# Optimization experiments

Measured on AMD Instinct MI355X. Metric: run time of the kernel, lower is better.

The kernel has to match this reference:

```python
import jax, jax.numpy as jnp
import numpy as np

N = 50000      # nodes
E = 800000     # edges (avg degree 16)
IN = 128
H = 128
OUT = 64
L = 3          # num GIN layers
G = 512        # graphs in batch
BN_EPS = 1e-5


def setup_inputs() -> dict:
    key = jax.random.key(0)
    ks = jax.random.split(key, 16)
    x = jax.random.normal(ks[0], (N, IN), dtype=jnp.float32)
    edge_index = jax.random.randint(ks[1], (2, E), 0, N, dtype=jnp.int64)
    batch = jnp.sort(jax.random.randint(ks[2], (N,), 0, G, dtype=jnp.int64))

    s_in = 1.0 / np.sqrt(IN)
    s_h = 1.0 / np.sqrt(H)
    # layer 0 has fan-in IN == H so we can stack all L layers uniformly
    conv_W1 = jax.random.normal(ks[3], (L, IN, H), dtype=jnp.float32) * s_in
    conv_b1 = jnp.zeros((L, H), dtype=jnp.float32)
    conv_gamma = jnp.ones((L, H), dtype=jnp.float32)
    conv_beta = jnp.zeros((L, H), dtype=jnp.float32)
    conv_W2 = jax.random.normal(ks[4], (L, H, H), dtype=jnp.float32) * s_h
    conv_b2 = jnp.zeros((L, H), dtype=jnp.float32)

    head_W1 = jax.random.normal(ks[5], (H, H), dtype=jnp.float32) * s_h
    head_b1 = jnp.zeros((H,), dtype=jnp.float32)
    head_W2 = jax.random.normal(ks[6], (H, OUT), dtype=jnp.float32) * s_h
    head_b2 = jnp.zeros((OUT,), dtype=jnp.float32)

    return dict(x=x, conv_W1=conv_W1, conv_b1=conv_b1, conv_gamma=conv_gamma,
                conv_beta=conv_beta, conv_W2=conv_W2, conv_b2=conv_b2,
                head_W1=head_W1, head_b1=head_b1, head_W2=head_W2,
                head_b2=head_b2, edge_index=edge_index, batch=batch)


def _mlp_bn(h, W1, b1, gamma, beta, W2, b2):
    # Linear -> BatchNorm (batch stats, biased var) -> ReLU -> Linear
    h = h @ W1 + b1
    mu = jnp.mean(h, axis=0)
    var = jnp.var(h, axis=0)
    h = (h - mu) * jax.lax.rsqrt(var + BN_EPS) * gamma + beta
    h = jax.nn.relu(h)
    return h @ W2 + b2


def reference(x, conv_W1, conv_b1, conv_gamma, conv_beta, conv_W2, conv_b2,
              head_W1, head_b1, head_W2, head_b2, edge_index, batch):
    src, dst = edge_index[0], edge_index[1]
    for l in range(L):
        # GINConv, eps=0: nn(x_i + sum_{j->i} x_j)
        agg = jax.ops.segment_sum(x[src], dst, num_segments=N)
        x = jax.nn.relu(_mlp_bn(x + agg, conv_W1[l], conv_b1[l],
                                conv_gamma[l], conv_beta[l],
                                conv_W2[l], conv_b2[l]))
    # global_add_pool -> [G, H]
    g = jax.ops.segment_sum(x, batch, num_segments=G)
    # head MLP (norm=None, dropout eval-mode identity)
    g = jax.nn.relu(g @ head_W1 + head_b1)
    return g @ head_W2 + head_b2
```

## Files before the change

kernel.cpp:

```cpp
#include <hip/hip_runtime.h>

#define N_NODES 50000
#define N_EDGES 800000
#define HDIM 128
#define ODIM 64
#define NLAYER 3
#define NGRAPH 512
#define BN_EPS 1e-5f
#define BCAP 48
#define NBUCKET 256
#define BRANGE 196
#define NBLK 782
#define GBLK 782
#define PROWS 64
#define HPITCH 136
#define TPITCH 136

#define SCAT_BLK 782
#define CVT_BLK 6250
#define CVTW_BLK 673

typedef __attribute__((ext_vector_type(8))) short short8;
typedef __attribute__((ext_vector_type(8))) unsigned short ushort8;
typedef __attribute__((ext_vector_type(4))) unsigned char uchar4x;
typedef __attribute__((ext_vector_type(2))) unsigned int uint2x;
typedef __attribute__((ext_vector_type(2))) float floatx2;
typedef __attribute__((ext_vector_type(4))) float floatx4;

static __device__ __forceinline__ unsigned short f2bf(float f) {
    union { float f; unsigned int u; } v; v.f = f;
    unsigned int r = v.u + 0x7FFFu + ((v.u >> 16) & 1u);
    return (unsigned short)(r >> 16);
}
static __device__ __forceinline__ float bf2f(unsigned short s) {
    union { unsigned int u; float f; } v; v.u = ((unsigned int)s) << 16;
    return v.f;
}
static __device__ __forceinline__ unsigned char f2e4(float f) {
    union { float f; unsigned int u; } v; v.f = f;
    unsigned char s = (unsigned char)((v.u >> 24) & 0x80u);
    float a = fabsf(f);
    if (a >= 448.f) return (unsigned char)(s | 0x7Eu);
    if (a < 0.015625f) return s;
    v.f = a;
    unsigned int r = v.u + 0x7FFFFu + ((v.u >> 20) & 1u);
    int e8 = (int)((r >> 23) & 0xFF) - 127 + 7;
    unsigned int man = (r >> 20) & 0x7u;
    if (e8 <= 0) return s;
    if (e8 > 15) return (unsigned char)(s | 0x7Eu);
    return (unsigned char)(s | ((unsigned)e8 << 3) | man);
}
static __device__ __forceinline__ void acc8_fp8(float* acc, const unsigned char* p) {
    uint2x u = *(const uint2x*)p;
    floatx2 p0 = __builtin_amdgcn_cvt_pk_f32_fp8(u[0], false);
    floatx2 p1 = __builtin_amdgcn_cvt_pk_f32_fp8(u[0], true);
    floatx2 p2 = __builtin_amdgcn_cvt_pk_f32_fp8(u[1], false);
    floatx2 p3 = __builtin_amdgcn_cvt_pk_f32_fp8(u[1], true);
    acc[0] += p0[0]; acc[1] += p0[1]; acc[2] += p1[0]; acc[3] += p1[1];
    acc[4] += p2[0]; acc[5] += p2[1]; acc[6] += p3[0]; acc[7] += p3[1];
}


__global__ __launch_bounds__(256) void k_prep(
    const int* __restrict__ src, const int* __restrict__ dst,
    unsigned int* __restrict__ bstore,
    unsigned int* __restrict__ prefW,
    int* __restrict__ vcnt,
    const float* __restrict__ x, unsigned char* __restrict__ xa,
    const float* __restrict__ W1, const float* __restrict__ W2,
    const float* __restrict__ hW1, const float* __restrict__ hW2,
    unsigned short* __restrict__ wtb,
    float* __restrict__ p64all)
{
    int b = blockIdx.x;
    int tid = threadIdx.x;
    if (b < SCAT_BLK) {
        __shared__ int hist[NBUCKET], pos[NBUCKET];
        __shared__ int sa[NBUCKET], sb[NBUCKET];
        __shared__ unsigned int sed[1024];
        hist[tid] = 0;
        __syncthreads();

        int base = (b * 256 + tid) * 4;
        bool valid = base < N_EDGES;
        unsigned int ev[4]; int bk[4];
        if (valid) {
            int4 s4 = *(const int4*)(src + base);
            int4 d4 = *(const int4*)(dst + base);
            ev[0] = (unsigned)s4.x | ((unsigned)d4.x << 16); bk[0] = d4.x / BRANGE;
            ev[1] = (unsigned)s4.y | ((unsigned)d4.y << 16); bk[1] = d4.y / BRANGE;
            ev[2] = (unsigned)s4.z | ((unsigned)d4.z << 16); bk[2] = d4.z / BRANGE;
            ev[3] = (unsigned)s4.w | ((unsigned)d4.w << 16); bk[3] = d4.w / BRANGE;
            atomicAdd(&hist[bk[0]], 1); atomicAdd(&hist[bk[1]], 1);
            atomicAdd(&hist[bk[2]], 1); atomicAdd(&hist[bk[3]], 1);
        }
        __syncthreads();

        sa[tid] = hist[tid];
        __syncthreads();
        int* pin = sa; int* pout = sb;
#pragma unroll
        for (int d = 1; d < NBUCKET; d <<= 1) {
            pout[tid] = pin[tid] + ((tid >= d) ? pin[tid - d] : 0);
            __syncthreads();
            int* t = pin; pin = pout; pout = t;
        }
        int excl = (tid > 0) ? pin[tid - 1] : 0;
        pos[tid] = excl;
        prefW[(size_t)b * NBUCKET + tid] = (unsigned int)excl;
        if (tid == NBUCKET - 1) vcnt[b] = pin[NBUCKET - 1];
        __syncthreads();

        if (valid) {
#pragma unroll
            for (int j = 0; j < 4; ++j) {
                int p = atomicAdd(&pos[bk[j]], 1);
                sed[p] = ev[j];
            }
        }
        __syncthreads();

        unsigned int* out = bstore + (size_t)b * 1024;
#pragma unroll
        for (int j = 0; j < 4; ++j) out[tid * 4 + j] = sed[tid * 4 + j];
    } else if (b < SCAT_BLK + CVT_BLK) {
        int i = (b - SCAT_BLK) * 256 + tid;
        if (i < N_NODES * HDIM / 4) {
            float4 v = ((const float4*)x)[i];
            uchar4x o;
            o[0] = f2e4(v.x); o[1] = f2e4(v.y); o[2] = f2e4(v.z); o[3] = f2e4(v.w);
            ((uchar4x*)xa)[i] = o;
        }
    } else {
        int idx = (b - SCAT_BLK - CVT_BLK) * 256 + tid;
        if (idx < 6 * HDIM * HDIM) {
            int mat = idx >> 14;
            int rem = idx & 16383;
            int k = rem >> 7, n = rem & 127;
            int l = mat >> 1;
            const float* W = (mat & 1) ? (W2 + l * HDIM * HDIM) : (W1 + l * HDIM * HDIM);
            wtb[mat * HDIM * HDIM + n * HDIM + k] = f2bf(W[k * HDIM + n]);
        } else if (idx < 7 * HDIM * HDIM) {
            int j = idx - 6 * HDIM * HDIM;
            int n = j >> 7, k = j & 127;
            wtb[idx] = f2bf(hW1[k * HDIM + n]);
        } else if (idx < 7 * HDIM * HDIM + ODIM * HDIM) {
            int j = idx - 7 * HDIM * HDIM;
            int n = j >> 7, k = j & 127;
            wtb[idx] = f2bf(hW2[k * ODIM + n]);
        } else if (idx < 7 * HDIM * HDIM + ODIM * HDIM + HDIM) {
            xa[(size_t)N_NODES * HDIM + (idx - 7 * HDIM * HDIM - ODIM * HDIM)] = 0;
        } else if (idx < 7 * HDIM * HDIM + ODIM * HDIM + HDIM + NLAYER * PROWS * 256) {
            p64all[idx - (7 * HDIM * HDIM + ODIM * HDIM + HDIM)] = 0.f;
        }
    }
}


__global__ __launch_bounds__(256) void k_bucket(
    const unsigned int* __restrict__ bstore,
    const unsigned int* __restrict__ prefW,
    const int* __restrict__ vcnt,
    int* __restrict__ cnt,
    unsigned short* __restrict__ colidx)
{
    __shared__ __align__(16) unsigned short lb[BRANGE * BCAP];
    __shared__ int lc[BRANGE];
    int k = blockIdx.x;
    int tid = threadIdx.x;
    if (tid < BRANGE) lc[tid] = 0;
    __syncthreads();

    for (int b = tid; b < SCAT_BLK; b += 256) {
        int s = (int)prefW[(size_t)b * NBUCKET + k];
        int e = (k == NBUCKET - 1) ? vcnt[b] : (int)prefW[(size_t)b * NBUCKET + k + 1];
        const unsigned int* seg = bstore + (size_t)b * 1024;
        for (int i = s; i < e; ++i) {
            unsigned int ed = seg[i];
            int ld = (int)(ed >> 16) - k * BRANGE;
            int p = atomicAdd(&lc[ld], 1);
            if (p < BCAP) lb[ld * BCAP + p] = (unsigned short)(ed & 0xFFFFu);
        }
    }
    __syncthreads();

    for (int d = tid; d < BRANGE; d += 256) {
        int deg = lc[d]; if (deg > BCAP) deg = BCAP;
        int end = (deg + 7) & ~7;
        for (int i = deg; i < end; ++i) lb[d * BCAP + i] = (unsigned short)N_NODES;
        cnt[k * BRANGE + d] = deg;
    }
    __syncthreads();

    short8* dst8 = (short8*)(colidx + (size_t)k * BRANGE * BCAP);
    const short8* src8 = (const short8*)lb;
    for (int i = tid; i < (BRANGE * BCAP) / 8; i += 256) dst8[i] = src8[i];
}


__global__ __launch_bounds__(512, 6) void k_gml(
    const unsigned char* __restrict__ x,
    const int* __restrict__ cnt,
    const unsigned short* __restrict__ colidx,
    const unsigned short* __restrict__ wt,
    const float* __restrict__ b1,
    unsigned short* __restrict__ hout,
    float* __restrict__ p64)
{
    __shared__ float s_sum[HDIM], s_sq[HDIM];
    __shared__ __align__(16) unsigned short yb[64 * TPITCH];
    int tid = threadIdx.x;
    if (tid < HDIM) { s_sum[tid] = 0.f; s_sq[tid] = 0.f; }
    int nbase = blockIdx.x * 64;

#pragma unroll
    for (int t = tid; t < 1024; t += 512) {
        int nl = t >> 4;
        int seg = (t & 15) * 8;
        int gnode = nbase + nl;
        float acc[8] = {0.f, 0.f, 0.f, 0.f, 0.f, 0.f, 0.f, 0.f};
        if (gnode < N_NODES) {
            acc8_fp8(acc, x + (size_t)gnode * HDIM + seg);
            int deg = cnt[gnode]; if (deg > BCAP) deg = BCAP;
            int e = gnode * BCAP;
            int end = e + ((deg + 7) & ~7);
            for (; e < end; e += 8) {
                ushort8 i0 = *(const ushort8*)(colidx + e);
                acc8_fp8(acc, x + (size_t)i0[0] * HDIM + seg);
                acc8_fp8(acc, x + (size_t)i0[1] * HDIM + seg);
                acc8_fp8(acc, x + (size_t)i0[2] * HDIM + seg);
                acc8_fp8(acc, x + (size_t)i0[3] * HDIM + seg);
                acc8_fp8(acc, x + (size_t)i0[4] * HDIM + seg);
                acc8_fp8(acc, x + (size_t)i0[5] * HDIM + seg);
                acc8_fp8(acc, x + (size_t)i0[6] * HDIM + seg);
                acc8_fp8(acc, x + (size_t)i0[7] * HDIM + seg);
            }
        }
        short8 o;
#pragma unroll
        for (int j = 0; j < 8; ++j) o[j] = (short)f2bf(acc[j]);
        *(short8*)&yb[nl * TPITCH + seg] = o;
    }
    __syncthreads();

    int wv = tid >> 6, lane = tid & 63;
    int m = lane & 15, quad = lane >> 4;
    int mrow = (wv & 3) * 16 + m;
    int ncol0 = (wv >> 2) * 64;

    short8 a[4];
#pragma unroll
    for (int kk = 0; kk < 4; ++kk)
        a[kk] = *(const short8*)&yb[mrow * TPITCH + kk * 32 + quad * 8];
    __syncthreads();

    floatx4 acc4[4];
#pragma unroll
    for (int nt = 0; nt < 4; ++nt) {
        floatx4 c = {0.f, 0.f, 0.f, 0.f};
#pragma unroll
        for (int kk = 0; kk < 4; ++kk) {
            short8 b = *(const short8*)(wt + (ncol0 + nt * 16 + m) * HDIM + kk * 32 + quad * 8);
            c = __builtin_amdgcn_mfma_f32_16x16x32_bf16(a[kk], b, c, 0, 0, 0);
        }
        acc4[nt] = c;
    }

    int lrow0 = (wv & 3) * 16 + quad * 4;
#pragma unroll
    for (int nt = 0; nt < 4; ++nt) {
        int n = ncol0 + nt * 16 + m;
        float bias = b1[n];
        float ssum = 0.f, ssq = 0.f;
#pragma unroll
        for (int r = 0; r < 4; ++r) {
            float val = acc4[nt][r] + bias;
            yb[(lrow0 + r) * TPITCH + n] = f2bf(val);
            if (nbase + lrow0 + r < N_NODES) { ssum += val; ssq += val * val; }
        }
        atomicAdd(&s_sum[n], ssum);
        atomicAdd(&s_sq[n], ssq);
    }
    __syncthreads();
    if (tid < HDIM) {
        int prow = (blockIdx.x & (PROWS - 1)) * 256;
        atomicAdd(&p64[prow + tid], s_sum[tid]);
        atomicAdd(&p64[prow + HDIM + tid], s_sq[tid]);
    }
    int lrow = tid >> 3, off = (tid & 7) * 16;
    int grow = nbase + lrow;
    if (grow < N_NODES) {
        *(short8*)(hout + (size_t)grow * HDIM + off) = *(const short8*)&yb[lrow * TPITCH + off];
        *(short8*)(hout + (size_t)grow * HDIM + off + 8) = *(const short8*)&yb[lrow * TPITCH + off + 8];
    }
}


__global__ __launch_bounds__(256) void k_mlp2(
    const unsigned short* __restrict__ hin,
    const float* __restrict__ p64,
    const float* __restrict__ gamma,
    const float* __restrict__ beta,
    const unsigned short* __restrict__ wt,
    const float* __restrict__ b2,
    unsigned char* __restrict__ xq,
    unsigned short* __restrict__ xbf,
    int last)
{
    __shared__ float red[256];
    __shared__ float s_scale[HDIM], s_shift[HDIM];
    __shared__ __align__(16) unsigned short tb[64 * TPITCH];
    int tid = threadIdx.x;

    {
        float s = 0.f;
#pragma unroll 8
        for (int i = 0; i < PROWS; ++i) s += p64[i * 256 + tid];
        red[tid] = s;
    }
    __syncthreads();
    if (tid < HDIM) {
        float mu = red[tid] * (1.f / N_NODES);
        float var = red[HDIM + tid] * (1.f / N_NODES) - mu * mu;
        float sc = gamma[tid] * rsqrtf(var + BN_EPS);
        s_scale[tid] = sc;
        s_shift[tid] = beta[tid] - mu * sc;
    }
    __syncthreads();

    int wv = tid >> 6, lane = tid & 63;
    int m = lane & 15, quad = lane >> 4;
    int row0 = blockIdx.x * 64 + wv * 16;
    int arow = row0 + m;

    short8 a[4];
    if (arow < N_NODES) {
#pragma unroll
        for (int kk = 0; kk < 4; ++kk) {
            short8 v = *(const short8*)(hin + (size_t)arow * HDIM + kk * 32 + quad * 8);
            int c0 = kk * 32 + quad * 8;
            short8 af;
#pragma unroll
            for (int j = 0; j < 8; ++j) {
                float f = fmaxf(bf2f((unsigned short)v[j]) * s_scale[c0 + j] + s_shift[c0 + j], 0.f);
                af[j] = (short)f2bf(f);
            }
            a[kk] = af;
        }
    } else {
#pragma unroll
        for (int kk = 0; kk < 4; ++kk) a[kk] = (short8)0;
    }

    floatx4 acc[8];
#pragma unroll
    for (int nt = 0; nt < 8; ++nt) {
        floatx4 c = {0.f, 0.f, 0.f, 0.f};
#pragma unroll
        for (int kk = 0; kk < 4; ++kk) {
            short8 b = *(const short8*)(wt + (nt * 16 + m) * HDIM + kk * 32 + quad * 8);
            c = __builtin_amdgcn_mfma_f32_16x16x32_bf16(a[kk], b, c, 0, 0, 0);
        }
        acc[nt] = c;
    }

    int lrow0 = wv * 16 + quad * 4;
#pragma unroll
    for (int nt = 0; nt < 8; ++nt) {
        int n = nt * 16 + m;
        float bias = b2[n];
#pragma unroll
        for (int r = 0; r < 4; ++r)
            tb[(lrow0 + r) * TPITCH + n] = f2bf(fmaxf(acc[nt][r] + bias, 0.f));
    }
    __syncthreads();
    int lrow = tid >> 2, offd = (tid & 3) * 32;
    int grow = blockIdx.x * 64 + lrow;
    if (grow < N_NODES) {
        if (last) {
#pragma unroll
            for (int i = 0; i < 4; ++i)
                *(short8*)(xbf + (size_t)grow * HDIM + offd + i * 8) =
                    *(const short8*)&tb[lrow * TPITCH + offd + i * 8];
        } else {
#pragma unroll
            for (int i = 0; i < 4; ++i) {
                short8 vv = *(const short8*)&tb[lrow * TPITCH + offd + i * 8];
                uchar4x qa, qb;
#pragma unroll
                for (int j = 0; j < 4; ++j) qa[j] = f2e4(bf2f((unsigned short)vv[j]));
#pragma unroll
                for (int j = 0; j < 4; ++j) qb[j] = f2e4(bf2f((unsigned short)vv[4 + j]));
                *(uchar4x*)(xq + (size_t)grow * HDIM + offd + i * 8) = qa;
                *(uchar4x*)(xq + (size_t)grow * HDIM + offd + i * 8 + 4) = qb;
            }
        }
    }
}


__global__ __launch_bounds__(256) void k_pool(
    const unsigned short* __restrict__ xf,
    const int* __restrict__ batch,
    unsigned short* __restrict__ g)
{
    __shared__ float red[16][HDIM];
    int gid = blockIdx.x;
    int tid = threadIdx.x;

    int lo = 0, hi = N_NODES;
    while (lo < hi) { int mid = (lo + hi) >> 1; if (batch[mid] < gid) lo = mid + 1; else hi = mid; }
    int start = lo;
    int lo2 = start, hi2 = N_NODES;
    while (lo2 < hi2) { int mid = (lo2 + hi2) >> 1; if (batch[mid] < gid + 1) lo2 = mid + 1; else hi2 = mid; }
    int end = lo2;

    int tsub = tid & 15, rgrp = tid >> 4;
    int seg = tsub * 8;
    float acc[8] = {0.f, 0.f, 0.f, 0.f, 0.f, 0.f, 0.f, 0.f};
    for (int r = start + rgrp; r < end; r += 16) {
        short8 v = *(const short8*)(xf + (size_t)r * HDIM + seg);
#pragma unroll
        for (int j = 0; j < 8; ++j) acc[j] += bf2f((unsigned short)v[j]);
    }
#pragma unroll
    for (int j = 0; j < 8; ++j) red[rgrp][seg + j] = acc[j];
    __syncthreads();
    if (tid < HDIM) {
        float s = 0.f;
#pragma unroll
        for (int i = 0; i < 16; ++i) s += red[i][tid];
        g[gid * HDIM + tid] = f2bf(s);
    }
}


__global__ __launch_bounds__(256) void k_head(
    const unsigned short* __restrict__ g,
    const unsigned short* __restrict__ w1t,
    const float* __restrict__ b1,
    const unsigned short* __restrict__ w2t,
    const float* __restrict__ b2,
    float* __restrict__ out)
{
    __shared__ unsigned short tb[64 * HPITCH];
    int tid = threadIdx.x;
    int wv = tid >> 6, lane = tid & 63;
    int m = lane & 15, quad = lane >> 4;
    int row0 = blockIdx.x * 64 + wv * 16;

    short8 a[4];
#pragma unroll
    for (int kk = 0; kk < 4; ++kk)
        a[kk] = *(const short8*)(g + (size_t)(row0 + m) * HDIM + kk * 32 + quad * 8);

#pragma unroll
    for (int nt = 0; nt < 8; ++nt) {
        floatx4 c = {0.f, 0.f, 0.f, 0.f};
#pragma unroll
        for (int kk = 0; kk < 4; ++kk) {
            short8 b = *(const short8*)(w1t + (nt * 16 + m) * HDIM + kk * 32 + quad * 8);
            c = __builtin_amdgcn_mfma_f32_16x16x32_bf16(a[kk], b, c, 0, 0, 0);
        }
        int n = nt * 16 + m;
        float bias = b1[n];
#pragma unroll
        for (int r = 0; r < 4; ++r) {
            int lrow = wv * 16 + quad * 4 + r;
            tb[lrow * HPITCH + n] = f2bf(fmaxf(c[r] + bias, 0.f));
        }
    }
    __syncthreads();

    short8 a2[4];
#pragma unroll
    for (int kk = 0; kk < 4; ++kk)
        a2[kk] = *(const short8*)&tb[(wv * 16 + m) * HPITCH + kk * 32 + quad * 8];

#pragma unroll
    for (int nt = 0; nt < 4; ++nt) {
        floatx4 c = {0.f, 0.f, 0.f, 0.f};
#pragma unroll
        for (int kk = 0; kk < 4; ++kk) {
            short8 b = *(const short8*)(w2t + (nt * 16 + m) * HDIM + kk * 32 + quad * 8);
            c = __builtin_amdgcn_mfma_f32_16x16x32_bf16(a2[kk], b, c, 0, 0, 0);
        }
        int n = nt * 16 + m;
        float bias = b2[n];
#pragma unroll
        for (int r = 0; r < 4; ++r) {
            int row = row0 + quad * 4 + r;
            out[(size_t)row * ODIM + n] = c[r] + bias;
        }
    }
}


extern "C" void kernel_launch(void* const* d_in, const int* in_sizes, int n_in,
                              void* d_out, int out_size, void* d_ws, size_t ws_size,
                              hipStream_t stream) {
    const float* x        = (const float*)d_in[0];
    const float* conv_W1  = (const float*)d_in[1];
    const float* conv_b1  = (const float*)d_in[2];
    const float* conv_g   = (const float*)d_in[3];
    const float* conv_be  = (const float*)d_in[4];
    const float* conv_W2  = (const float*)d_in[5];
    const float* conv_b2  = (const float*)d_in[6];
    const float* head_W1  = (const float*)d_in[7];
    const float* head_b1  = (const float*)d_in[8];
    const float* head_W2  = (const float*)d_in[9];
    const float* head_b2  = (const float*)d_in[10];
    const int*   edges    = (const int*)d_in[11];
    const int*   batch    = (const int*)d_in[12];

    char* ws = (char*)d_ws;
    int*            cnt    = (int*)(ws + 0);
    unsigned short* colidx = (unsigned short*)(ws + 200704);
    unsigned short* wtb    = (unsigned short*)(ws + 5017600);
    float*          part64 = (float*)(ws + 5263360);
    unsigned int*   bstore = (unsigned int*)(ws + 5459968);
    unsigned int*   prefW  = (unsigned int*)(ws + 8663040);
    int*            vcnt   = (int*)(ws + 9463808);
    unsigned short* gbuf   = (unsigned short*)(ws + 9467008);
    unsigned char*  xa     = (unsigned char*)(ws + 9598080);
    unsigned short* xb     = (unsigned short*)(ws + 15998208);
    (void)in_sizes; (void)n_in; (void)out_size; (void)ws_size;


    k_prep<<<SCAT_BLK + CVT_BLK + CVTW_BLK, 256, 0, stream>>>(
        edges, edges + N_EDGES, bstore, prefW, vcnt, x, xa,
        conv_W1, conv_W2, head_W1, head_W2, wtb, part64);
    k_bucket<<<NBUCKET, 256, 0, stream>>>(bstore, prefW, vcnt, cnt, colidx);

    for (int l = 0; l < NLAYER; ++l) {
        k_gml<<<GBLK, 512, 0, stream>>>(xa, cnt, colidx,
                                        wtb + (2 * l) * HDIM * HDIM,
                                        conv_b1 + l * HDIM, xb,
                                        part64 + (size_t)l * PROWS * 256);
        k_mlp2<<<NBLK, 256, 0, stream>>>(xb, part64 + (size_t)l * PROWS * 256,
                                         conv_g + l * HDIM, conv_be + l * HDIM,
                                         wtb + (2 * l + 1) * HDIM * HDIM,
                                         conv_b2 + l * HDIM, xa, xb,
                                         (l == NLAYER - 1) ? 1 : 0);
    }

    k_pool<<<NGRAPH, 256, 0, stream>>>(xb, batch, gbuf);
    k_head<<<NGRAPH / 64, 256, 0, stream>>>(gbuf, wtb + 6 * HDIM * HDIM, head_b1,
                                            wtb + 7 * HDIM * HDIM, head_b2,
                                            (float*)d_out);
}
```

Before: 361.6 us.

## Fuse global add pooling into last MLP2 layer via atomic segment sums

```diff
diff --git a/kernel.cpp b/kernel.cpp
--- a/kernel.cpp
+++ b/kernel.cpp
@@ -18,7 +18,7 @@
 
 #define SCAT_BLK 782
 #define CVT_BLK 6250
-#define CVTW_BLK 673
+#define CVTW_BLK 929
 
 typedef __attribute__((ext_vector_type(8))) short short8;
 typedef __attribute__((ext_vector_type(8))) unsigned short ushort8;
@@ -70,7 +70,8 @@
     const float* __restrict__ W1, const float* __restrict__ W2,
     const float* __restrict__ hW1, const float* __restrict__ hW2,
     unsigned short* __restrict__ wtb,
-    float* __restrict__ p64all)
+    float* __restrict__ p64all,
+    float* __restrict__ gpool)
 {
     int b = blockIdx.x;
     int tid = threadIdx.x;
@@ -152,6 +153,8 @@
             xa[(size_t)N_NODES * HDIM + (idx - 7 * HDIM * HDIM - ODIM * HDIM)] = 0;
         } else if (idx < 7 * HDIM * HDIM + ODIM * HDIM + HDIM + NLAYER * PROWS * 256) {
             p64all[idx - (7 * HDIM * HDIM + ODIM * HDIM + HDIM)] = 0.f;
+        } else if (idx < 7 * HDIM * HDIM + ODIM * HDIM + HDIM + NLAYER * PROWS * 256 + NGRAPH * HDIM) {
+            gpool[idx - (7 * HDIM * HDIM + ODIM * HDIM + HDIM + NLAYER * PROWS * 256)] = 0.f;
         }
     }
 }
@@ -304,14 +307,20 @@
     const unsigned short* __restrict__ wt,
     const float* __restrict__ b2,
     unsigned char* __restrict__ xq,
-    unsigned short* __restrict__ xbf,
+    float* __restrict__ gpool,
+    const int* __restrict__ batch,
     int last)
 {
     __shared__ float red[256];
     __shared__ float s_scale[HDIM], s_shift[HDIM];
+    __shared__ int sgid[64];
     __shared__ __align__(16) unsigned short tb[64 * TPITCH];
     int tid = threadIdx.x;
 
+    if (last && tid < 64) {
+        int gr = blockIdx.x * 64 + tid;
+        sgid[tid] = (gr < N_NODES) ? batch[gr] : -1;
+    }
     {
         float s = 0.f;
 #pragma unroll 8
@@ -374,15 +383,24 @@
             tb[(lrow0 + r) * TPITCH + n] = f2bf(fmaxf(acc[nt][r] + bias, 0.f));
     }
     __syncthreads();
-    int lrow = tid >> 2, offd = (tid & 3) * 32;
-    int grow = blockIdx.x * 64 + lrow;
-    if (grow < N_NODES) {
-        if (last) {
-#pragma unroll
-            for (int i = 0; i < 4; ++i)
-                *(short8*)(xbf + (size_t)grow * HDIM + offd + i * 8) =
-                    *(const short8*)&tb[lrow * TPITCH + offd + i * 8];
-        } else {
+    if (last) {
+        int col = tid & 127, half = tid >> 7;
+        int gprev = -1; float s = 0.f;
+        int r0 = half * 32;
+        for (int r = r0; r < r0 + 32; ++r) {
+            if (blockIdx.x * 64 + r >= N_NODES) break;
+            int gg = sgid[r];
+            if (gg != gprev) {
+                if (gprev >= 0) atomicAdd(&gpool[(size_t)gprev * HDIM + col], s);
+                s = 0.f; gprev = gg;
+            }
+            s += bf2f(tb[r * TPITCH + col]);
+        }
+        if (gprev >= 0) atomicAdd(&gpool[(size_t)gprev * HDIM + col], s);
+    } else {
+        int lrow = tid >> 2, offd = (tid & 3) * 32;
+        int grow = blockIdx.x * 64 + lrow;
+        if (grow < N_NODES) {
 #pragma unroll
             for (int i = 0; i < 4; ++i) {
                 short8 vv = *(const short8*)&tb[lrow * TPITCH + offd + i * 8];
@@ -399,44 +417,8 @@
 }
 
 
-__global__ __launch_bounds__(256) void k_pool(
-    const unsigned short* __restrict__ xf,
-    const int* __restrict__ batch,
-    unsigned short* __restrict__ g)
-{
-    __shared__ float red[16][HDIM];
-    int gid = blockIdx.x;
-    int tid = threadIdx.x;
-
-    int lo = 0, hi = N_NODES;
-    while (lo < hi) { int mid = (lo + hi) >> 1; if (batch[mid] < gid) lo = mid + 1; else hi = mid; }
-    int start = lo;
-    int lo2 = start, hi2 = N_NODES;
-    while (lo2 < hi2) { int mid = (lo2 + hi2) >> 1; if (batch[mid] < gid + 1) lo2 = mid + 1; else hi2 = mid; }
-    int end = lo2;
-
-    int tsub = tid & 15, rgrp = tid >> 4;
-    int seg = tsub * 8;
-    float acc[8] = {0.f, 0.f, 0.f, 0.f, 0.f, 0.f, 0.f, 0.f};
-    for (int r = start + rgrp; r < end; r += 16) {
-        short8 v = *(const short8*)(xf + (size_t)r * HDIM + seg);
-#pragma unroll
-        for (int j = 0; j < 8; ++j) acc[j] += bf2f((unsigned short)v[j]);
-    }
-#pragma unroll
-    for (int j = 0; j < 8; ++j) red[rgrp][seg + j] = acc[j];
-    __syncthreads();
-    if (tid < HDIM) {
-        float s = 0.f;
-#pragma unroll
-        for (int i = 0; i < 16; ++i) s += red[i][tid];
-        g[gid * HDIM + tid] = f2bf(s);
-    }
-}
-
-
 __global__ __launch_bounds__(256) void k_head(
-    const unsigned short* __restrict__ g,
+    const float* __restrict__ g,
     const unsigned short* __restrict__ w1t,
     const float* __restrict__ b1,
     const unsigned short* __restrict__ w2t,
@@ -451,8 +433,17 @@
 
     short8 a[4];
 #pragma unroll
-    for (int kk = 0; kk < 4; ++kk)
-        a[kk] = *(const short8*)(g + (size_t)(row0 + m) * HDIM + kk * 32 + quad * 8);
+    for (int kk = 0; kk < 4; ++kk) {
+        const float* gp = g + (size_t)(row0 + m) * HDIM + kk * 32 + quad * 8;
+        float4 f0 = *(const float4*)gp;
+        float4 f1 = *(const float4*)(gp + 4);
+        short8 af;
+        af[0] = (short)f2bf(f0.x); af[1] = (short)f2bf(f0.y);
+        af[2] = (short)f2bf(f0.z); af[3] = (short)f2bf(f0.w);
+        af[4] = (short)f2bf(f1.x); af[5] = (short)f2bf(f1.y);
+        af[6] = (short)f2bf(f1.z); af[7] = (short)f2bf(f1.w);
+        a[kk] = af;
+    }
 
 #pragma unroll
     for (int nt = 0; nt < 8; ++nt) {
@@ -521,15 +512,15 @@
     unsigned int*   bstore = (unsigned int*)(ws + 5459968);
     unsigned int*   prefW  = (unsigned int*)(ws + 8663040);
     int*            vcnt   = (int*)(ws + 9463808);
-    unsigned short* gbuf   = (unsigned short*)(ws + 9467008);
-    unsigned char*  xa     = (unsigned char*)(ws + 9598080);
-    unsigned short* xb     = (unsigned short*)(ws + 15998208);
+    float*          gpool  = (float*)(ws + 9467008);
+    unsigned char*  xa     = (unsigned char*)(ws + 9729152);
+    unsigned short* xb     = (unsigned short*)(ws + 16129280);
     (void)in_sizes; (void)n_in; (void)out_size; (void)ws_size;
 
 
     k_prep<<<SCAT_BLK + CVT_BLK + CVTW_BLK, 256, 0, stream>>>(
         edges, edges + N_EDGES, bstore, prefW, vcnt, x, xa,
-        conv_W1, conv_W2, head_W1, head_W2, wtb, part64);
+        conv_W1, conv_W2, head_W1, head_W2, wtb, part64, gpool);
     k_bucket<<<NBUCKET, 256, 0, stream>>>(bstore, prefW, vcnt, cnt, colidx);
 
     for (int l = 0; l < NLAYER; ++l) {
@@ -540,12 +531,11 @@
         k_mlp2<<<NBLK, 256, 0, stream>>>(xb, part64 + (size_t)l * PROWS * 256,
                                          conv_g + l * HDIM, conv_be + l * HDIM,
                                          wtb + (2 * l + 1) * HDIM * HDIM,
-                                         conv_b2 + l * HDIM, xa, xb,
+                                         conv_b2 + l * HDIM, xa, gpool, batch,
                                          (l == NLAYER - 1) ? 1 : 0);
     }
 
-    k_pool<<<NGRAPH, 256, 0, stream>>>(xb, batch, gbuf);
-    k_head<<<NGRAPH / 64, 256, 0, stream>>>(gbuf, wtb + 6 * HDIM * HDIM, head_b1,
+    k_head<<<NGRAPH / 64, 256, 0, stream>>>(gpool, wtb + 6 * HDIM * HDIM, head_b1,
                                             wtb + 7 * HDIM * HDIM, head_b2,
                                             (float*)d_out);
 }
```

Result: faster. 345.4 us (-4.5%).
